# Optimization experiments

Measured on AMD Instinct MI355X. Metric: run time of the kernel, lower is better.

## Reference

```python
import jax, jax.numpy as jnp
import numpy as np

NUM_EXPERTS = 64
HIDDEN = 4096
TOP_K = 2
B, S = 4, 4096


def setup_inputs() -> dict:
    key = jax.random.key(0)
    k1, k2 = jax.random.split(key)
    hidden_states = jax.random.normal(k1, (B, S, HIDDEN), dtype=jnp.float32)
    W = jax.random.normal(k2, (NUM_EXPERTS, HIDDEN), dtype=jnp.float32) * 0.02
    return {"hidden_states": hidden_states, "W": W}


def reference(hidden_states, W):
    # router logits: [B, S, E]
    logits = jnp.einsum("bsh,eh->bse", hidden_states, W)
    flat = logits.reshape(-1, NUM_EXPERTS)  # [T, E]
    # top-k routing (z-loss / aux-loss do not change forward values; they only
    # inject gradients via the custom autograd function in the torch original)
    scores, top_indices = jax.lax.top_k(flat, TOP_K)  # [T, K] each
    return (scores.reshape(B, S, TOP_K), top_indices.reshape(B, S, TOP_K))
```

## Files before the change

### kernel.cpp

```cpp
#include <hip/hip_runtime.h>
#include <hip/hip_bf16.h>
#include <math.h>

#define NUM_EXPERTS 64
#define HIDDEN      4096
#define T_TOKENS    16384

using short8 = __attribute__((ext_vector_type(8))) short;
using f32x4  = __attribute__((ext_vector_type(4))) float;

__device__ __forceinline__ unsigned pack_pair(float f0, float f1, unsigned& lopk) {
    __hip_bfloat162 h2 = __float22bfloat162_rn(make_float2(f0, f1));
    unsigned hb; __builtin_memcpy(&hb, &h2, 4);
    float h0 = __builtin_bit_cast(float, hb << 16);
    float h1 = __builtin_bit_cast(float, hb & 0xffff0000u);
    __hip_bfloat162 l2 = __float22bfloat162_rn(make_float2(f0 - h0, f1 - h1));
    unsigned lb; __builtin_memcpy(&lb, &l2, 4);
    lopk = lb;
    return hb;
}
__device__ __forceinline__ void split8(const float4 a, const float4 b, uint4& hi, uint4& lo) {
    hi.x = pack_pair(a.x, a.y, lo.x);
    hi.y = pack_pair(a.z, a.w, lo.y);
    hi.z = pack_pair(b.x, b.y, lo.z);
    hi.w = pack_pair(b.z, b.w, lo.w);
}

#define MFMA(a, b, c) __builtin_amdgcn_mfma_f32_16x16x32_bf16((a), (b), (c), 0, 0, 0)

#define GLOAD16(g_, l_)                                                        \
    __builtin_amdgcn_global_load_lds(                                          \
        (__attribute__((address_space(1))) unsigned*)(void*)(g_),              \
        (__attribute__((address_space(3))) unsigned*)(void*)(l_), 16, 0, 0)

__global__ __launch_bounds__(256) void w_split_kernel(
    const float* __restrict__ W, unsigned char* __restrict__ ws)
{
    const int j  = blockIdx.x * 256 + threadIdx.x;
    const int l  = j & 63;
    const int nt = (j >> 6) & 3;
    const int t  = j >> 8;
    const int e  = nt * 16 + (l & 15);
    const int k0 = t * 32 + ((l >> 4) & 3) * 8;
    const float* p = W + (size_t)e * HIDDEN + k0;
    float4 w0 = *reinterpret_cast<const float4*>(p);
    float4 w1 = *reinterpret_cast<const float4*>(p + 4);
    uint4 hi, lo;
    split8(w0, w1, hi, lo);
    *reinterpret_cast<uint4*>(ws + (size_t)j * 16)            = hi;
    *reinterpret_cast<uint4*>(ws + 524288 + (size_t)j * 16)   = lo;
}


#define LOAD_W(dst, t_) do {                                                   \
    const unsigned char* pW_ = wsHi + (size_t)(tBase + (t_)) * 4096 + laneOff; \
    _Pragma("unroll")                                                          \
    for (int nt_ = 0; nt_ < 4; ++nt_) {                                        \
        dst[nt_]     = *reinterpret_cast<const uint4*>(pW_ + nt_ * 1024);      \
        dst[nt_ + 4] = *reinterpret_cast<const uint4*>(pW_ + 524288 + nt_ * 1024); \
    } } while (0)

#define STAGE_A(b_, t_) do {                                                   \
    unsigned char* ld_ = smem + (size_t)w * 16384 + (b_) * 8192;               \
    const float* g0_ = aBase + (size_t)(t_) * 32;                              \
    _Pragma("unroll")                                                          \
    for (int mt_ = 0; mt_ < 4; ++mt_) {                                        \
        const float* g_ = g0_ + (size_t)mt_ * 16 * HIDDEN;                     \
        GLOAD16(g_,     ld_ + mt_ * 2048);                                     \
        GLOAD16(g_ + 4, ld_ + mt_ * 2048 + 1024);                              \
    } } while (0)

#define ITER(t_, bufA_, wCur_, wNxt_) do {                                     \
    asm volatile("s_waitcnt vmcnt(8)" ::: "memory");                           \
    __builtin_amdgcn_sched_barrier(0);                                         \
    const unsigned char* ls_ = smem + (size_t)w * 16384 + (bufA_) * 8192 + laneOff; \
    float4 q_[4][2];                                                           \
    _Pragma("unroll")                                                          \
    for (int mt_ = 0; mt_ < 4; ++mt_) {                                        \
        q_[mt_][0] = *reinterpret_cast<const float4*>(ls_ + mt_ * 2048);       \
        q_[mt_][1] = *reinterpret_cast<const float4*>(ls_ + mt_ * 2048 + 1024);\
    }                                                                          \
    asm volatile("s_waitcnt lgkmcnt(0)" ::: "memory");                         \
    __builtin_amdgcn_sched_barrier(0);                                         \
    if ((t_) + 1 < 16) LOAD_W(wNxt_, (t_) + 1);                                \
    if ((t_) + 2 < 16) STAGE_A(bufA_, (t_) + 2);                               \
    _Pragma("unroll")                                                          \
    for (int mt_ = 0; mt_ < 4; ++mt_) {                                        \
        uint4 hi_, lo_;                                                        \
        split8(q_[mt_][0], q_[mt_][1], hi_, lo_);                              \
        short8 ah_ = __builtin_bit_cast(short8, hi_);                          \
        short8 al_ = __builtin_bit_cast(short8, lo_);                          \
        _Pragma("unroll")                                                      \
        for (int nt_ = 0; nt_ < 4; ++nt_) {                                    \
            short8 wh_ = __builtin_bit_cast(short8, wCur_[nt_]);               \
            short8 wl_ = __builtin_bit_cast(short8, wCur_[nt_ + 4]);           \
            acc[mt_][nt_] = MFMA(ah_, wh_, acc[mt_][nt_]);                     \
            acc[mt_][nt_] = MFMA(ah_, wl_, acc[mt_][nt_]);                     \
            acc[mt_][nt_] = MFMA(al_, wh_, acc[mt_][nt_]);                     \
        } }                                                                    \
} while (0)

__global__ __launch_bounds__(512, 2) void router_mfma_topk(
    const float* __restrict__ A,
    const unsigned char* __restrict__ wsHi,
    float* __restrict__ out)
{
    __shared__ unsigned char smem[131072];

    const int tid  = threadIdx.x;
    const int lane = tid & 63;
    const int w    = tid >> 6;
    const int tok0 = blockIdx.x * 64;
    const int tBase = w * 16;

    const float* aBase = A + (size_t)(tok0 + (lane & 15)) * HIDDEN
                           + w * 512 + ((lane >> 4) & 3) * 8;
    const int laneOff = lane * 16;

    f32x4 acc[4][4];
#pragma unroll
    for (int mt = 0; mt < 4; ++mt)
#pragma unroll
        for (int nt = 0; nt < 4; ++nt) acc[mt][nt] = (f32x4){0.f, 0.f, 0.f, 0.f};

    uint4 wX[8], wY[8];

    LOAD_W(wX, 0);
    STAGE_A(0, 0);
    STAGE_A(1, 1);

    ITER( 0, 0, wX, wY);  ITER( 1, 1, wY, wX);
    ITER( 2, 0, wX, wY);  ITER( 3, 1, wY, wX);
    ITER( 4, 0, wX, wY);  ITER( 5, 1, wY, wX);
    ITER( 6, 0, wX, wY);  ITER( 7, 1, wY, wX);
    ITER( 8, 0, wX, wY);  ITER( 9, 1, wY, wX);
    ITER(10, 0, wX, wY);  ITER(11, 1, wY, wX);
    ITER(12, 0, wX, wY);  ITER(13, 1, wY, wX);
    ITER(14, 0, wX, wY);  ITER(15, 1, wY, wX);

    f32x4 (*part)[4][4][64] = reinterpret_cast<f32x4 (*)[4][4][64]>(smem);

    __syncthreads();
    if (w < 4) {
#pragma unroll
        for (int mt = 0; mt < 4; ++mt)
#pragma unroll
            for (int nt = 0; nt < 4; ++nt) part[w][mt][nt][lane] = acc[mt][nt];
    }
    __syncthreads();
    if (w >= 4) {
#pragma unroll
        for (int mt = 0; mt < 4; ++mt)
#pragma unroll
            for (int nt = 0; nt < 4; ++nt)
                part[w - 4][mt][nt][lane] = part[w - 4][mt][nt][lane] + acc[mt][nt];
    }
    __syncthreads();

    if (w < 4) {
        f32x4 s[4];
#pragma unroll
        for (int nt = 0; nt < 4; ++nt) {
            s[nt] = part[0][w][nt][lane];
#pragma unroll
            for (int q = 1; q < 4; ++q) s[nt] = s[nt] + part[q][w][nt][lane];
        }

        const int eBase = lane & 15;
#pragma unroll
        for (int r = 0; r < 4; ++r) {
            float b1 = s[0][r]; int i1 = eBase;
            float b2 = -INFINITY; int i2 = 0;
#pragma unroll
            for (int nt = 1; nt < 4; ++nt) {
                float v = s[nt][r];
                int   e = nt * 16 + eBase;
                if (v > b1)      { b2 = b1; i2 = i1; b1 = v; i1 = e; }
                else if (v > b2) { b2 = v;  i2 = e; }
            }
#pragma unroll
            for (int m = 1; m <= 8; m <<= 1) {
                float o1 = __shfl_xor(b1, m); int oi1 = __shfl_xor(i1, m);
                float o2 = __shfl_xor(b2, m); int oi2 = __shfl_xor(i2, m);
                float n1, c, n2; int ni1, ci, ni2;
                if (o1 > b1 || (o1 == b1 && oi1 < i1)) { n1 = o1; ni1 = oi1; c = b1; ci = i1; }
                else                                   { n1 = b1; ni1 = i1;  c = o1; ci = oi1; }
                if (b2 > o2 || (b2 == o2 && i2 < oi2)) { n2 = b2; ni2 = i2; }
                else                                   { n2 = o2; ni2 = oi2; }
                if (c > n2 || (c == n2 && ci < ni2))   { n2 = c;  ni2 = ci; }
                b1 = n1; i1 = ni1; b2 = n2; i2 = ni2;
            }
            if ((lane & 15) == 0) {
                const int tok = tok0 + w * 16 + (lane >> 4) * 4 + r;
                out[(size_t)tok * 2 + 0] = b1;
                out[(size_t)tok * 2 + 1] = b2;
                out[(size_t)2 * T_TOKENS + (size_t)tok * 2 + 0] = (float)i1;
                out[(size_t)2 * T_TOKENS + (size_t)tok * 2 + 1] = (float)i2;
            }
        }
    }
}

extern "C" void kernel_launch(void* const* d_in, const int* in_sizes, int n_in,
                              void* d_out, int out_size, void* d_ws, size_t ws_size,
                              hipStream_t stream) {
    const float* A = (const float*)d_in[0];
    const float* W = (const float*)d_in[1];
    float* out = (float*)d_out;
    unsigned char* ws = (unsigned char*)d_ws;

    w_split_kernel<<<dim3(128), dim3(256), 0, stream>>>(W, ws);
    router_mfma_topk<<<dim3(T_TOKENS / 64), dim3(512), 0, stream>>>(A, ws, out);
}
```

Baseline: 64.19 us.

## Split-K router GEMM with 128-token tiles and separate top-k combine kernel

```diff
diff --git a/kernel.cpp b/kernel.cpp
--- a/kernel.cpp
+++ b/kernel.cpp
@@ -32,6 +32,10 @@
     __builtin_amdgcn_global_load_lds(                                          \
         (__attribute__((address_space(1))) unsigned*)(void*)(g_),              \
         (__attribute__((address_space(3))) unsigned*)(void*)(l_), 16, 0, 0)
+
+#define WAITVM(n_)  asm volatile("s_waitcnt vmcnt(" #n_ ")" ::: "memory")
+#define WAITLG()    asm volatile("s_waitcnt lgkmcnt(0)" ::: "memory")
+#define SB()        __builtin_amdgcn_sched_barrier(0)
 
 __global__ __launch_bounds__(256) void w_split_kernel(
     const float* __restrict__ W, unsigned char* __restrict__ ws)
@@ -60,74 +64,86 @@
         dst[nt_ + 4] = *reinterpret_cast<const uint4*>(pW_ + 524288 + nt_ * 1024); \
     } } while (0)
 
-#define STAGE_A(b_, t_) do {                                                   \
-    unsigned char* ld_ = smem + (size_t)w * 16384 + (b_) * 8192;               \
+#define STAGE_A8(b_, t_) do {                                                  \
+    unsigned char* ld_ = smem + (size_t)w * 32768 + (b_) * 16384;              \
     const float* g0_ = aBase + (size_t)(t_) * 32;                              \
     _Pragma("unroll")                                                          \
-    for (int mt_ = 0; mt_ < 4; ++mt_) {                                        \
+    for (int mt_ = 0; mt_ < 8; ++mt_) {                                        \
         const float* g_ = g0_ + (size_t)mt_ * 16 * HIDDEN;                     \
         GLOAD16(g_,     ld_ + mt_ * 2048);                                     \
         GLOAD16(g_ + 4, ld_ + mt_ * 2048 + 1024);                              \
     } } while (0)
 
-#define ITER(t_, bufA_, wCur_, wNxt_) do {                                     \
-    asm volatile("s_waitcnt vmcnt(8)" ::: "memory");                           \
-    __builtin_amdgcn_sched_barrier(0);                                         \
-    const unsigned char* ls_ = smem + (size_t)w * 16384 + (bufA_) * 8192 + laneOff; \
-    float4 q_[4][2];                                                           \
-    _Pragma("unroll")                                                          \
-    for (int mt_ = 0; mt_ < 4; ++mt_) {                                        \
-        q_[mt_][0] = *reinterpret_cast<const float4*>(ls_ + mt_ * 2048);       \
-        q_[mt_][1] = *reinterpret_cast<const float4*>(ls_ + mt_ * 2048 + 1024);\
-    }                                                                          \
-    asm volatile("s_waitcnt lgkmcnt(0)" ::: "memory");                         \
-    __builtin_amdgcn_sched_barrier(0);                                         \
-    if ((t_) + 1 < 16) LOAD_W(wNxt_, (t_) + 1);                                \
-    if ((t_) + 2 < 16) STAGE_A(bufA_, (t_) + 2);                               \
-    _Pragma("unroll")                                                          \
-    for (int mt_ = 0; mt_ < 4; ++mt_) {                                        \
+#define SUB_READ(q_, ls_, mt0_) do {                                           \
+    _Pragma("unroll")                                                          \
+    for (int i_ = 0; i_ < 4; ++i_) {                                           \
+        q_[i_][0] = *reinterpret_cast<const float4*>((ls_) + (mt0_ + i_) * 2048);        \
+        q_[i_][1] = *reinterpret_cast<const float4*>((ls_) + (mt0_ + i_) * 2048 + 1024); \
+    } } while (0)
+
+#define SUB_MFMA(q_, mt0_, wb_) do {                                           \
+    _Pragma("unroll")                                                          \
+    for (int i_ = 0; i_ < 4; ++i_) {                                           \
         uint4 hi_, lo_;                                                        \
-        split8(q_[mt_][0], q_[mt_][1], hi_, lo_);                              \
+        split8(q_[i_][0], q_[i_][1], hi_, lo_);                                \
         short8 ah_ = __builtin_bit_cast(short8, hi_);                          \
         short8 al_ = __builtin_bit_cast(short8, lo_);                          \
         _Pragma("unroll")                                                      \
         for (int nt_ = 0; nt_ < 4; ++nt_) {                                    \
-            short8 wh_ = __builtin_bit_cast(short8, wCur_[nt_]);               \
-            short8 wl_ = __builtin_bit_cast(short8, wCur_[nt_ + 4]);           \
-            acc[mt_][nt_] = MFMA(ah_, wh_, acc[mt_][nt_]);                     \
-            acc[mt_][nt_] = MFMA(ah_, wl_, acc[mt_][nt_]);                     \
-            acc[mt_][nt_] = MFMA(al_, wh_, acc[mt_][nt_]);                     \
-        } }                                                                    \
+            short8 wh_ = __builtin_bit_cast(short8, wb_[nt_]);                 \
+            short8 wl_ = __builtin_bit_cast(short8, wb_[nt_ + 4]);             \
+            acc[mt0_ + i_][nt_] = MFMA(ah_, wh_, acc[mt0_ + i_][nt_]);         \
+            acc[mt0_ + i_][nt_] = MFMA(ah_, wl_, acc[mt0_ + i_][nt_]);         \
+            acc[mt0_ + i_][nt_] = MFMA(al_, wh_, acc[mt0_ + i_][nt_]);         \
+        } } } while (0)
+
+#define ITER_BODY(t_, buf_, wCur_, wNxt_) do {                                 \
+    SB();                                                                      \
+    const unsigned char* ls_ = smem + (size_t)w * 32768 + (buf_) * 16384 + laneOff; \
+    float4 qA_[4][2];                                                          \
+    SUB_READ(qA_, ls_, 0);                                                     \
+    WAITLG(); SB();                                                            \
+    if ((t_) + 1 < 16) LOAD_W(wNxt_, (t_) + 1);                                \
+    SUB_MFMA(qA_, 0, wCur_);                                                   \
+    float4 qB_[4][2];                                                          \
+    SUB_READ(qB_, ls_, 4);                                                     \
+    WAITLG(); SB();                                                            \
+    if ((t_) + 2 < 16) STAGE_A8(buf_, (t_) + 2);                               \
+    SUB_MFMA(qB_, 4, wCur_);                                                   \
 } while (0)
 
-__global__ __launch_bounds__(512, 2) void router_mfma_topk(
+#define ITER(t_, buf_, wCur_, wNxt_)      do { WAITVM(16); ITER_BODY(t_, buf_, wCur_, wNxt_); } while (0)
+#define ITER_LAST(t_, buf_, wCur_, wNxt_) do { WAITVM(0);  ITER_BODY(t_, buf_, wCur_, wNxt_); } while (0)
+
+__global__ __launch_bounds__(256, 1) void router_gemm_partial(
     const float* __restrict__ A,
     const unsigned char* __restrict__ wsHi,
-    float* __restrict__ out)
+    float* __restrict__ partG)
 {
     __shared__ unsigned char smem[131072];
 
     const int tid  = threadIdx.x;
     const int lane = tid & 63;
     const int w    = tid >> 6;
-    const int tok0 = blockIdx.x * 64;
-    const int tBase = w * 16;
+    const int ky   = blockIdx.y;
+    const int tok0 = blockIdx.x * 128;
+    const int tBase = ky * 64 + w * 16;
 
     const float* aBase = A + (size_t)(tok0 + (lane & 15)) * HIDDEN
-                           + w * 512 + ((lane >> 4) & 3) * 8;
+                           + ky * 2048 + w * 512 + ((lane >> 4) & 3) * 8;
     const int laneOff = lane * 16;
 
-    f32x4 acc[4][4];
-#pragma unroll
-    for (int mt = 0; mt < 4; ++mt)
+    f32x4 acc[8][4];
+#pragma unroll
+    for (int mt = 0; mt < 8; ++mt)
 #pragma unroll
         for (int nt = 0; nt < 4; ++nt) acc[mt][nt] = (f32x4){0.f, 0.f, 0.f, 0.f};
 
     uint4 wX[8], wY[8];
 
     LOAD_W(wX, 0);
-    STAGE_A(0, 0);
-    STAGE_A(1, 1);
+    STAGE_A8(0, 0);
+    STAGE_A8(1, 1);
 
     ITER( 0, 0, wX, wY);  ITER( 1, 1, wY, wX);
     ITER( 2, 0, wX, wY);  ITER( 3, 1, wY, wX);
@@ -136,69 +152,63 @@
     ITER( 8, 0, wX, wY);  ITER( 9, 1, wY, wX);
     ITER(10, 0, wX, wY);  ITER(11, 1, wY, wX);
     ITER(12, 0, wX, wY);  ITER(13, 1, wY, wX);
-    ITER(14, 0, wX, wY);  ITER(15, 1, wY, wX);
-
-    f32x4 (*part)[4][4][64] = reinterpret_cast<f32x4 (*)[4][4][64]>(smem);
+    ITER(14, 0, wX, wY);  ITER_LAST(15, 1, wY, wX);
+
+    f32x4 (*part)[8][4][64] = reinterpret_cast<f32x4 (*)[8][4][64]>(smem);
 
     __syncthreads();
-    if (w < 4) {
-#pragma unroll
-        for (int mt = 0; mt < 4; ++mt)
-#pragma unroll
-            for (int nt = 0; nt < 4; ++nt) part[w][mt][nt][lane] = acc[mt][nt];
-    }
+#pragma unroll
+    for (int mt = 0; mt < 8; ++mt)
+#pragma unroll
+        for (int nt = 0; nt < 4; ++nt) part[w][mt][nt][lane] = acc[mt][nt];
     __syncthreads();
-    if (w >= 4) {
-#pragma unroll
-        for (int mt = 0; mt < 4; ++mt)
-#pragma unroll
-            for (int nt = 0; nt < 4; ++nt)
-                part[w - 4][mt][nt][lane] = part[w - 4][mt][nt][lane] + acc[mt][nt];
-    }
-    __syncthreads();
-
-    if (w < 4) {
-        f32x4 s[4];
+
+#pragma unroll
+    for (int j = 0; j < 2; ++j) {
+        const int mt = 2 * w + j;
 #pragma unroll
         for (int nt = 0; nt < 4; ++nt) {
-            s[nt] = part[0][w][nt][lane];
-#pragma unroll
-            for (int q = 1; q < 4; ++q) s[nt] = s[nt] + part[q][w][nt][lane];
-        }
-
-        const int eBase = lane & 15;
-#pragma unroll
-        for (int r = 0; r < 4; ++r) {
-            float b1 = s[0][r]; int i1 = eBase;
-            float b2 = -INFINITY; int i2 = 0;
-#pragma unroll
-            for (int nt = 1; nt < 4; ++nt) {
-                float v = s[nt][r];
-                int   e = nt * 16 + eBase;
-                if (v > b1)      { b2 = b1; i2 = i1; b1 = v; i1 = e; }
-                else if (v > b2) { b2 = v;  i2 = e; }
-            }
-#pragma unroll
-            for (int m = 1; m <= 8; m <<= 1) {
-                float o1 = __shfl_xor(b1, m); int oi1 = __shfl_xor(i1, m);
-                float o2 = __shfl_xor(b2, m); int oi2 = __shfl_xor(i2, m);
-                float n1, c, n2; int ni1, ci, ni2;
-                if (o1 > b1 || (o1 == b1 && oi1 < i1)) { n1 = o1; ni1 = oi1; c = b1; ci = i1; }
-                else                                   { n1 = b1; ni1 = i1;  c = o1; ci = oi1; }
-                if (b2 > o2 || (b2 == o2 && i2 < oi2)) { n2 = b2; ni2 = i2; }
-                else                                   { n2 = o2; ni2 = oi2; }
-                if (c > n2 || (c == n2 && ci < ni2))   { n2 = c;  ni2 = ci; }
-                b1 = n1; i1 = ni1; b2 = n2; i2 = ni2;
-            }
-            if ((lane & 15) == 0) {
-                const int tok = tok0 + w * 16 + (lane >> 4) * 4 + r;
-                out[(size_t)tok * 2 + 0] = b1;
-                out[(size_t)tok * 2 + 1] = b2;
-                out[(size_t)2 * T_TOKENS + (size_t)tok * 2 + 0] = (float)i1;
-                out[(size_t)2 * T_TOKENS + (size_t)tok * 2 + 1] = (float)i2;
+            f32x4 s = part[0][mt][nt][lane];
+#pragma unroll
+            for (int q = 1; q < 4; ++q) s = s + part[q][mt][nt][lane];
+            const int e = nt * 16 + (lane & 15);
+#pragma unroll
+            for (int r = 0; r < 4; ++r) {
+                const int tok = tok0 + mt * 16 + (lane >> 4) * 4 + r;
+                partG[((size_t)ky * T_TOKENS + tok) * 64 + e] = s[r];
             }
         }
     }
+}
+
+__global__ __launch_bounds__(64) void combine_topk(
+    const float* __restrict__ partG,
+    float* __restrict__ out)
+{
+    const int tok = blockIdx.x * 64 + threadIdx.x;
+    const float4* p0 = reinterpret_cast<const float4*>(partG + (size_t)tok * 64);
+    const float4* p1 = reinterpret_cast<const float4*>(partG + ((size_t)T_TOKENS + tok) * 64);
+
+    float s[64];
+#pragma unroll
+    for (int i = 0; i < 16; ++i) {
+        float4 a = p0[i], b = p1[i];
+        s[4*i+0] = a.x + b.x; s[4*i+1] = a.y + b.y;
+        s[4*i+2] = a.z + b.z; s[4*i+3] = a.w + b.w;
+    }
+
+    float b1 = -INFINITY, b2 = -INFINITY;
+    int i1 = 0, i2 = 0;
+#pragma unroll
+    for (int e = 0; e < NUM_EXPERTS; ++e) {
+        float v = s[e];
+        if (v > b1)      { b2 = b1; i2 = i1; b1 = v; i1 = e; }
+        else if (v > b2) { b2 = v;  i2 = e; }
+    }
+    out[(size_t)tok * 2 + 0] = b1;
+    out[(size_t)tok * 2 + 1] = b2;
+    out[(size_t)2 * T_TOKENS + (size_t)tok * 2 + 0] = (float)i1;
+    out[(size_t)2 * T_TOKENS + (size_t)tok * 2 + 1] = (float)i2;
 }
 
 extern "C" void kernel_launch(void* const* d_in, const int* in_sizes, int n_in,
@@ -208,7 +218,9 @@
     const float* W = (const float*)d_in[1];
     float* out = (float*)d_out;
     unsigned char* ws = (unsigned char*)d_ws;
+    float* partG = reinterpret_cast<float*>(ws + (1 << 20));
 
     w_split_kernel<<<dim3(128), dim3(256), 0, stream>>>(W, ws);
-    router_mfma_topk<<<dim3(T_TOKENS / 64), dim3(512), 0, stream>>>(A, ws, out);
-}
+    router_gemm_partial<<<dim3(T_TOKENS / 128, 2), dim3(256), 0, stream>>>(A, ws, partG);
+    combine_topk<<<dim3(T_TOKENS / 64), dim3(64), 0, stream>>>(partG, out);
+}
```

Measured after the change: 61.11 us, median of 2. 4.8% less time.
